# Kernel optimization log

Hardware: AMD Instinct MI355X
Metric: run time of the kernel (lower is better)

Reference implementation:

```python
import jax, jax.numpy as jnp
import numpy as np

N_DESC = 2
CC_ITERS = 500  # kornia.contrib.connected_components(num_iterations=500)
MIN_PTS = 10


def find_contours(img):
    """Faithful jax port of findContours: pad, kornia connected_components,
    3x3 Laplacian boundary mask, crop. img: [B,1,H,W] binary float32."""
    B, _, H, W = img.shape
    I = jnp.pad(img, ((0, 0), (0, 0), (1, 1), (1, 1)))
    mask = I == 1.0
    # kornia CC: labels initialized to global linear index, propagated by masked 3x3 max-pool
    idx = jnp.arange(B * (H + 2) * (W + 2), dtype=jnp.float32).reshape(B, 1, H + 2, W + 2)
    out0 = jnp.where(mask, idx, 0.0)

    def body(_, o):
        p = jax.lax.reduce_window(o, -jnp.inf, jax.lax.max,
                                  (1, 1, 3, 3), (1, 1, 1, 1), 'SAME')
        return jnp.where(mask, p, 0.0)

    cc = jax.lax.fori_loop(0, CC_ITERS, body, out0)[:, :, 1:-1, 1:-1]
    kern = jnp.array([[1., 1., 1.], [1., -8., 1.], [1., 1., 1.]], dtype=jnp.float32).reshape(1, 1, 3, 3)
    lap = jax.lax.conv_general_dilated(I, kern, (1, 1), 'SAME')
    boundary = (lap < 0).astype(jnp.float32)[:, :, 1:-1, 1:-1]
    return boundary * cc


find_contours = jax.jit(find_contours)


def _sample_stats(cimg, N):
    """Per-image: unique labels (including 0, as in the original), polar-angle
    sort, Fourier descriptor base A_k = sqrt(a^2+b^2)/len with a,b = sums of
    real/imag FFT coefficients / (k*pi). Returns (centers, A) or None."""
    labels = np.unique(cimg)
    if labels.size == 1:
        return None
    centers, As = [], []
    ks = np.arange(1, N + 1, dtype=np.float64)
    for lb in labels:
        pts = np.argwhere(cimg == lb).astype(np.float64)  # (n, 2) row, col
        c = pts.mean(axis=0)
        ang = np.arctan2(pts[:, 1] - c[1], pts[:, 0] - c[0])
        pts = pts[np.argsort(ang, kind='stable')]
        if pts.shape[0] < MIN_PTS:
            continue
        z = pts[:, 0] + 1j * pts[:, 1]
        Fz = np.fft.fft(z)
        a = Fz.real.sum()
        b = Fz.imag.sum()
        A = np.sqrt((a / (ks * np.pi)) ** 2 + (b / (ks * np.pi)) ** 2) / pts.shape[0]
        centers.append(c)
        As.append(A)
    if len(centers) == 0:
        return None
    return np.stack(centers), np.stack(As)


def _compute_S(pred_c, tgt_c, N):
    """S = sum over batch of sum |A_pred[match] - A_gt| (weight-independent part).
    The descriptor is A * 0.5*w^2 + log(1+w^2); the log term cancels in the
    matched absolute difference, so loss = 0.5*w^2 * S exactly."""
    S = 0.0
    for b in range(pred_c.shape[0]):
        sp = _sample_stats(pred_c[b, 0], N)
        st = _sample_stats(tgt_c[b, 0], N)
        if sp is None or st is None:
            continue
        pc, pA = sp
        tc, tA = st
        if tc.shape[0] <= pc.shape[0]:
            d = ((tc[:, None, :] - pc[None, :, :]) ** 2).sum(-1)
            m = d.argmin(axis=1)
            S += np.abs(pA[m] - tA).sum()
        else:
            d = ((pc[:, None, :] - tc[None, :, :]) ** 2).sum(-1)
            m = d.argmin(axis=1)
            S += np.abs(tA[m] - pA).sum()
    return np.float32(S)


def setup_inputs() -> dict:
    key = jax.random.key(0)
    k1, k2, k3 = jax.random.split(key, 3)
    B, H, W = 8, 512, 512
    # low-frequency logits -> realistic building-like blobs after thresholding
    low_p = jax.random.normal(k1, (B, 1, 16, 16), dtype=jnp.float32)
    pred_seg = jax.image.resize(low_p, (B, 1, H, W), method='bilinear') * 4.0
    low_t = jax.random.normal(k2, (B, 1, 16, 16), dtype=jnp.float32)
    target_label = (jax.image.resize(low_t, (B, 1, H, W), method='bilinear') > 0).astype(jnp.float32)
    descriptors_weight = jax.random.uniform(k3, (), dtype=jnp.float32) + 0.5
    return {"pred_seg": pred_seg, "target_label": target_label,
            "descriptors_weight": descriptors_weight}


def reference(pred_seg, target_label, descriptors_weight):
    N = N_DESC
    pred = (jax.nn.sigmoid(pred_seg) > 0.5).astype(jnp.float32)
    tgt = target_label if target_label.ndim == 4 else target_label[:, None]
    pred_contours = np.asarray(find_contours(pred))
    tgt_contours = np.asarray(find_contours(tgt))
    S = _compute_S(pred_contours, tgt_contours, N)
    # descriptor = A * (1/2 * w^2) + log(1 + w^2); log term cancels in |diff|
    return jnp.asarray(S, jnp.float32) * (0.5 * descriptors_weight ** 2)
```

## Files before the change

### kernel.cpp

```cpp
#include <hip/hip_runtime.h>

typedef unsigned int u32;
typedef unsigned long long u64;

#define BN 8
#define NIMG 16
#define NPIMG (512*512)
#define NPIXC (NIMG*NPIMG)
#define PP (514*514)
#define CAP 8192u
#define SLOT0 8192
#define NSLOT 8193
#define NDN (NIMG*NSLOT)
#define TOTR 66977792u
#define MAXL 512
#define PROP_ITERS 500
#define LH 64

#define TILE_W 96
#define TILE_H 64
#define HALO 16
#define CF4 32
#define NSTRIP 8
#define SROWS 12
#define TPC 6
#define TPR 8
#define TPT (TPR*TPC)
#define PROPBLOCKS (NIMG*TPT)

__device__ __forceinline__ u32 hashL(u32 L) { return (L * 2654435761u) >> 19; }
__device__ __forceinline__ u32 hashS(u32 L) { return (L * 2654435761u) >> 26; }

__device__ __forceinline__ u64 encAng(double a) {
  u64 u = (u64)__double_as_longlong(a);
  return (u >> 63) ? ~u : (u | 0x8000000000000000ull);
}

__device__ __forceinline__ float fmax3(float a, float b, float c) {
  return fmaxf(a, fmaxf(b, c));
}

__device__ __forceinline__ float4 horizf4(float4 M, int tx) {
  float Lw = __shfl_up(M.w, 1);
  float Rx = __shfl_down(M.x, 1);
  if (tx == 0) Lw = 0.f;
  if (tx == CF4 - 1) Rx = 0.f;
  float4 hh;
  hh.x = fmax3(Lw, M.x, M.y);
  hh.y = fmax3(M.x, M.y, M.z);
  hh.z = fmax3(M.y, M.z, M.w);
  hh.w = fmax3(M.z, M.w, Rx);
  return hh;
}

__global__ __launch_bounds__(256) void k_prop(const float* __restrict__ src,
                                              float* __restrict__ dst,
                                              const float* __restrict__ pred,
                                              const float* __restrict__ tgt,
                                              int niter, int first) {
  __shared__ float4 hTopS[2][NSTRIP][CF4];
  __shared__ float4 hBotS[2][NSTRIP][CF4];
  __shared__ int s_flag;
  const int tid = threadIdx.x;
  const int bx = blockIdx.x;
  const int j = bx >> 3;
  const int img = ((bx & 7) << 1) + (j >= TPT ? 1 : 0);
  const int tt = (j >= TPT) ? (j - TPT) : j;
  const int tyT = tt / TPC, txT = tt % TPC;
  const int tx = tid & 31, sy = tid >> 5;
  const int gr0 = tyT * TILE_H - HALO + sy * SROWS;
  const int gc = txT * TILE_W - HALO + tx * 4;
  const bool gcok = (gc >= 0 && gc < 512);

  float4 cur[SROWS];
  if (first) {
    const int f = img >> 3, b = img & 7;
    const float* fb = (f == 0 ? pred : tgt) + b * NPIMG;
#pragma unroll
    for (int r = 0; r < SROWS; ++r) {
      float4 v = make_float4(0.f, 0.f, 0.f, 0.f);
      int gr = gr0 + r;
      if (gcok && gr >= 0 && gr < 512) {
        float4 x = *(const float4*)(fb + gr * 512 + gc);
        float lb = (float)(b * PP + (gr + 1) * 514 + (gc + 1));
        bool mx, my, mz, mw;
        if (f == 0) { mx = x.x > 0.f; my = x.y > 0.f; mz = x.z > 0.f; mw = x.w > 0.f; }
        else        { mx = x.x == 1.f; my = x.y == 1.f; mz = x.z == 1.f; mw = x.w == 1.f; }
        v.x = mx ? lb : 0.f;
        v.y = my ? lb + 1.f : 0.f;
        v.z = mz ? lb + 2.f : 0.f;
        v.w = mw ? lb + 3.f : 0.f;
      }
      cur[r] = v;
    }
  } else {
    const float* ibase = src + img * NPIMG;
#pragma unroll
    for (int r = 0; r < SROWS; ++r) {
      float4 v = make_float4(0.f, 0.f, 0.f, 0.f);
      int gr = gr0 + r;
      if (gcok && gr >= 0 && gr < 512)
        v = *(const float4*)(ibase + gr * 512 + gc);
      cur[r] = v;
    }
  }

  bool changed = false;
  for (int itr = 0; itr < niter; ++itr) {
    const int p = itr & 1;
    const bool chk = (p == 1);
    float4 h[SROWS];
#pragma unroll
    for (int r = 0; r < SROWS; ++r) h[r] = horizf4(cur[r], tx);
    hTopS[p][sy][tx] = h[0];
    hBotS[p][sy][tx] = h[SROWS - 1];
    if (chk && tid == 0) s_flag = 0;
    __syncthreads();
    float4 zero = make_float4(0.f, 0.f, 0.f, 0.f);
    float4 hm = (sy > 0) ? hBotS[p][sy - 1][tx] : zero;
    float4 below = (sy < NSTRIP - 1) ? hTopS[p][sy + 1][tx] : zero;
#pragma unroll
    for (int r = 0; r < SROWS; ++r) {
      float4 hc = h[r];
      float4 hp = (r == SROWS - 1) ? below : h[r + 1];
      float4 o = cur[r], v;
      v.x = (o.x > 0.f) ? fmax3(hm.x, hc.x, hp.x) : 0.f;
      v.y = (o.y > 0.f) ? fmax3(hm.y, hc.y, hp.y) : 0.f;
      v.z = (o.z > 0.f) ? fmax3(hm.z, hc.z, hp.z) : 0.f;
      v.w = (o.w > 0.f) ? fmax3(hm.w, hc.w, hp.w) : 0.f;
      if (chk)
        changed = changed || (v.x != o.x) || (v.y != o.y) || (v.z != o.z) || (v.w != o.w);
      cur[r] = v;
      hm = hc;
    }
    if (chk) {
      if (changed) s_flag = 1;
      __syncthreads();
      if (s_flag == 0) break;
      changed = false;
    }
  }

  if (tx >= 4 && tx <= 27 && gc < 512) {
    float* obase = dst + img * NPIMG;
#pragma unroll
    for (int r = 0; r < SROWS; ++r) {
      int er = sy * SROWS + r;
      if (er >= HALO && er < HALO + TILE_H)
        *(float4*)(obase + (gr0 + r) * 512 + gc) = cur[r];
    }
  }
}

__global__ __launch_bounds__(256) void k_cimgcount(const float* __restrict__ V,
                                                   float* __restrict__ Cm,
                                                   u32* __restrict__ key, u32* __restrict__ cnt,
                                                   u32* __restrict__ sr, u32* __restrict__ sc) {
  __shared__ u32 hl[LH], hn[LH], hr[LH], hc2[LH];
  __shared__ u32 s_n, s_r, s_c;
  const int tid = threadIdx.x;
  for (int e = tid; e < LH; e += 256) { hl[e] = 0; hn[e] = 0; hr[e] = 0; hc2[e] = 0; }
  if (tid == 0) { s_n = 0; s_r = 0; s_c = 0; }
  __syncthreads();
  int i = blockIdx.x * 256 + tid;
  int img = i >> 18, q = i & (NPIMG - 1);
  int r = q >> 9, c = q & 511;
  const float* base = V + img * NPIMG;
  float v = base[q];
  float out = 0.f;
  if (v > 0.f) {
    bool z = (r == 0) || (r == 511) || (c == 0) || (c == 511);
    if (!z) {
      float mn = base[q - 513];
      mn = fminf(mn, base[q - 512]); mn = fminf(mn, base[q - 511]);
      mn = fminf(mn, base[q - 1]);   mn = fminf(mn, base[q + 1]);
      mn = fminf(mn, base[q + 511]); mn = fminf(mn, base[q + 512]);
      mn = fminf(mn, base[q + 513]);
      z = (mn == 0.f);
    }
    if (z) out = v;
  }
  Cm[i] = out;
  if (out != 0.f) {
    u32 L = (u32)out;
    u32 h = hashS(L);
    bool ins = false;
    for (u32 pr = 0; pr < LH; ++pr) {
      u32 e = (h + pr) & (LH - 1);
      u32 k = atomicCAS(&hl[e], 0u, L);
      if (k == 0u || k == L) {
        atomicAdd(&hn[e], 1u); atomicAdd(&hr[e], (u32)r); atomicAdd(&hc2[e], (u32)c);
        ins = true; break;
      }
    }
    if (!ins) {
      u32 hg = hashL(L), slot = 0xFFFFFFFFu;
      for (u32 pr = 0; pr < CAP; ++pr) {
        u32 k = key[img * CAP + hg];
        if (k == L) { slot = hg; break; }
        if (k == 0u) {
          u32 old = atomicCAS(&key[img * CAP + hg], 0u, L);
          if (old == 0u || old == L) { slot = hg; break; }
        }
        hg = (hg + 1) & (CAP - 1);
      }
      if (slot != 0xFFFFFFFFu) {
        u32 s = (u32)img * NSLOT + slot;
        atomicAdd(&cnt[s], 1u); atomicAdd(&sr[s], (u32)r); atomicAdd(&sc[s], (u32)c);
      }
    }
    atomicAdd(&s_n, 1u); atomicAdd(&s_r, (u32)r); atomicAdd(&s_c, (u32)c);
  }
  __syncthreads();
  int im = (blockIdx.x * 256) >> 18;
  for (int e = tid; e < LH; e += 256) {
    u32 L = hl[e];
    if (L == 0u) continue;
    u32 hg = hashL(L), slot = 0xFFFFFFFFu;
    for (u32 pr = 0; pr < CAP; ++pr) {
      u32 k = key[im * CAP + hg];
      if (k == L) { slot = hg; break; }
      if (k == 0u) {
        u32 old = atomicCAS(&key[im * CAP + hg], 0u, L);
        if (old == 0u || old == L) { slot = hg; break; }
      }
      hg = (hg + 1) & (CAP - 1);
    }
    if (slot != 0xFFFFFFFFu) {
      u32 s = (u32)im * NSLOT + slot;
      atomicAdd(&cnt[s], hn[e]); atomicAdd(&sr[s], hr[e]); atomicAdd(&sc[s], hc2[e]);
    }
  }
  if (tid == 0 && s_n) {
    u32 s = (u32)im * NSLOT + SLOT0;
    atomicAdd(&cnt[s], s_n); atomicAdd(&sr[s], s_r); atomicAdd(&sc[s], s_c);
  }
}

__global__ __launch_bounds__(256) void k_compact(const u32* __restrict__ key,
                                                 const u32* __restrict__ cnt,
                                                 const u32* __restrict__ sr, const u32* __restrict__ sc,
                                                 u32* __restrict__ nlab, u32* __restrict__ labD,
                                                 u32* __restrict__ cntD, u32* __restrict__ srD,
                                                 u32* __restrict__ scD, u32* __restrict__ slotD) {
  int i = blockIdx.x * 256 + threadIdx.x;
  if (i >= NDN) return;
  int img = i / NSLOT, s = i - img * NSLOT;
  u32 L, n, a, b2;
  if (s < (int)CAP) {
    L = key[img * CAP + s];
    if (L == 0u) return;
    n = cnt[img * NSLOT + s];
    a = sr[img * NSLOT + s]; b2 = sc[img * NSLOT + s];
  } else {
    u32 nn = cnt[img * NSLOT + SLOT0];
    n = NPIMG - nn;
    if (n == 0u) return;
    L = 0u;
    a = TOTR - sr[img * NSLOT + SLOT0]; b2 = TOTR - sc[img * NSLOT + SLOT0];
  }
  u32 j = atomicAdd(&nlab[img], 1u);
  if (j < MAXL) {
    labD[img * MAXL + j] = L; cntD[img * MAXL + j] = n;
    srD[img * MAXL + j] = a;  scD[img * MAXL + j] = b2;
    slotD[img * MAXL + j] = (u32)s;
  }
}

__global__ __launch_bounds__(256) void k_angle(const float* __restrict__ Cm,
                                               const u32* __restrict__ key, const u32* __restrict__ cnt,
                                               const u32* __restrict__ sr, const u32* __restrict__ sc,
                                               u64* __restrict__ amin) {
  __shared__ u32 asl[LH];
  __shared__ u64 amn[LH];
  __shared__ u64 wmin[4];
  const int tid = threadIdx.x;
  for (int e = tid; e < LH; e += 256) { asl[e] = 0; amn[e] = ~0ull; }
  __syncthreads();
  int i = blockIdx.x * 256 + tid;
  int img = i >> 18, q = i & (NPIMG - 1);
  int r = q >> 9, c = q & 511;
  float v = Cm[i];
  u64 e0 = ~0ull;
  if (v == 0.f) {
    u32 base = (u32)img * NSLOT + SLOT0;
    u32 n0 = NPIMG - cnt[base];
    double cr = (double)(TOTR - sr[base]) / (double)n0;
    double cc = (double)(TOTR - sc[base]) / (double)n0;
    e0 = encAng(atan2((double)c - cc, (double)r - cr));
  } else {
    u32 L = (u32)v;
    u32 h = hashL(L);
    for (u32 pr = 0; pr < CAP && key[img * CAP + h] != L; ++pr) h = (h + 1) & (CAP - 1);
    u32 s = (u32)img * NSLOT + h;
    u32 n = cnt[s];
    double cr = (double)sr[s] / (double)n;
    double cc = (double)sc[s] / (double)n;
    u64 enc = encAng(atan2((double)c - cc, (double)r - cr));
    u32 kk = h + 1, hh = hashS(kk);
    bool ins = false;
    for (u32 pr = 0; pr < LH; ++pr) {
      u32 e = (hh + pr) & (LH - 1);
      u32 k = atomicCAS(&asl[e], 0u, kk);
      if (k == 0u || k == kk) { atomicMin(&amn[e], enc); ins = true; break; }
    }
    if (!ins) atomicMin(&amin[s], enc);
  }
  for (int o = 32; o > 0; o >>= 1) {
    u64 other = __shfl_xor(e0, o, 64);
    e0 = other < e0 ? other : e0;
  }
  int lane = tid & 63, wid = tid >> 6;
  if (lane == 0) wmin[wid] = e0;
  __syncthreads();
  int im = (blockIdx.x * 256) >> 18;
  if (tid == 0) {
    u64 m = wmin[0];
    for (int k = 1; k < 4; ++k) m = wmin[k] < m ? wmin[k] : m;
    if (m != ~0ull) atomicMin(&amin[(u32)im * NSLOT + SLOT0], m);
  }
  for (int e = tid; e < LH; e += 256)
    if (asl[e]) atomicMin(&amin[(u32)im * NSLOT + (asl[e] - 1)], amn[e]);
}

__global__ __launch_bounds__(256) void k_idx(const float* __restrict__ Cm,
                                             const u32* __restrict__ key, const u32* __restrict__ cnt,
                                             const u32* __restrict__ sr, const u32* __restrict__ sc,
                                             const u64* __restrict__ amin, u32* __restrict__ imin) {
  __shared__ u32 isl[LH];
  __shared__ u32 imn[LH];
  const int tid = threadIdx.x;
  for (int e = tid; e < LH; e += 256) { isl[e] = 0; imn[e] = 0xFFFFFFFFu; }
  __syncthreads();
  int i = blockIdx.x * 256 + tid;
  int img = i >> 18, q = i & (NPIMG - 1);
  int r = q >> 9, c = q & 511;
  float v = Cm[i];
  u32 sl; double cr, cc;
  if (v == 0.f) {
    sl = SLOT0;
    u32 s = (u32)img * NSLOT + SLOT0;
    u32 n0 = NPIMG - cnt[s];
    cr = (double)(TOTR - sr[s]) / (double)n0;
    cc = (double)(TOTR - sc[s]) / (double)n0;
  } else {
    u32 L = (u32)v;
    u32 h = hashL(L);
    for (u32 pr = 0; pr < CAP && key[img * CAP + h] != L; ++pr) h = (h + 1) & (CAP - 1);
    sl = h;
    u32 s = (u32)img * NSLOT + h;
    u32 n = cnt[s];
    cr = (double)sr[s] / (double)n;
    cc = (double)sc[s] / (double)n;
  }
  u64 e = encAng(atan2((double)c - cc, (double)r - cr));
  if (e == amin[(u32)img * NSLOT + sl]) {
    u32 kk = sl + 1, hh = hashS(kk);
    bool ins = false;
    for (u32 pr = 0; pr < LH; ++pr) {
      u32 e2 = (hh + pr) & (LH - 1);
      u32 k = atomicCAS(&isl[e2], 0u, kk);
      if (k == 0u || k == kk) { atomicMin(&imn[e2], (u32)q); ins = true; break; }
    }
    if (!ins) atomicMin(&imin[(u32)img * NSLOT + sl], (u32)q);
  }
  __syncthreads();
  int im = (blockIdx.x * 256) >> 18;
  for (int e2 = tid; e2 < LH; e2 += 256)
    if (isl[e2]) atomicMin(&imin[(u32)im * NSLOT + (isl[e2] - 1)], imn[e2]);
}

__global__ __launch_bounds__(256) void k_match(const u32* __restrict__ nlab,
                                               const u32* __restrict__ labD, const u32* __restrict__ cntD,
                                               const u32* __restrict__ srD, const u32* __restrict__ scD,
                                               const u32* __restrict__ slotD, const u32* __restrict__ imin,
                                               const float* __restrict__ wp, float* __restrict__ out) {
  __shared__ u32 lbl[2][MAXL];
  __shared__ double cx[2][MAXL], cy[2][MAXL], Rr[2][MAXL];
  __shared__ int nlist[2];
  __shared__ double wsum[4];
  const int tid = threadIdx.x;
  double S = 0.0;
  for (int b = 0; b < BN; ++b) {
    __syncthreads();
    if (tid == 0) { nlist[0] = nlist[1] = 0; }
    __syncthreads();
    int tot[2];
    for (int f = 0; f < 2; ++f) {
      int t = f * BN + b;
      int ntot = (int)nlab[t];
      tot[f] = ntot;
      int nl = ntot > MAXL ? MAXL : ntot;
      for (int s2 = tid; s2 < nl; s2 += 256) {
        u32 n = cntD[t * MAXL + s2];
        if (n < 10u) continue;
        int j = atomicAdd(&nlist[f], 1);
        lbl[f][j] = labD[t * MAXL + s2];
        cx[f][j] = (double)srD[t * MAXL + s2] / (double)n;
        cy[f][j] = (double)scD[t * MAXL + s2] / (double)n;
        u32 pi = imin[t * NSLOT + slotD[t * MAXL + s2]];
        double r0 = (double)(pi >> 9), c0 = (double)(pi & 511u);
        Rr[f][j] = sqrt(r0 * r0 + c0 * c0);
      }
    }
    __syncthreads();
    int np = nlist[0], nt = nlist[1];
    bool valid = (tot[0] >= 2) && (np >= 1) && (tot[1] >= 2) && (nt >= 1);
    if (valid) {
      u32 ml[2][2]; double mx[2][2], my[2][2], mr[2][2]; int rk[2][2]; int nh[2];
      for (int f = 0; f < 2; ++f) {
        int n = f ? nt : np;
        nh[f] = 0;
        for (int i = tid; i < n; i += 256) {
          int k = nh[f]++;
          u32 L = lbl[f][i];
          ml[f][k] = L; mx[f][k] = cx[f][i]; my[f][k] = cy[f][i]; mr[f][k] = Rr[f][i];
          int rr = 0;
          for (int j = 0; j < n; ++j) rr += (lbl[f][j] < L) ? 1 : 0;
          rk[f][k] = rr;
        }
      }
      __syncthreads();
      for (int f = 0; f < 2; ++f)
        for (int k = 0; k < nh[f]; ++k) {
          int rr = rk[f][k];
          lbl[f][rr] = ml[f][k]; cx[f][rr] = mx[f][k];
          cy[f][rr] = my[f][k];  Rr[f][rr] = mr[f][k];
        }
      __syncthreads();
      if (nt <= np) {
        for (int j = tid; j < nt; j += 256) {
          int m = 0; double bd = 1e300;
          double tx0 = cx[1][j], ty0 = cy[1][j];
          for (int i2 = 0; i2 < np; ++i2) {
            double dx = tx0 - cx[0][i2], dy = ty0 - cy[0][i2];
            double d = dx * dx + dy * dy;
            if (d < bd) { bd = d; m = i2; }
          }
          S += fabs(Rr[0][m] - Rr[1][j]);
        }
      } else {
        for (int i2 = tid; i2 < np; i2 += 256) {
          int m = 0; double bd = 1e300;
          double px0 = cx[0][i2], py0 = cy[0][i2];
          for (int j = 0; j < nt; ++j) {
            double dx = px0 - cx[1][j], dy = py0 - cy[1][j];
            double d = dx * dx + dy * dy;
            if (d < bd) { bd = d; m = j; }
          }
          S += fabs(Rr[1][m] - Rr[0][i2]);
        }
      }
    }
  }
  for (int o = 32; o > 0; o >>= 1) S += __shfl_xor(S, o, 64);
  int lane = tid & 63, wid = tid >> 6;
  if (lane == 0) wsum[wid] = S;
  __syncthreads();
  if (tid == 0) {
    double total = wsum[0] + wsum[1] + wsum[2] + wsum[3];
    total *= (1.5 / 3.14159265358979323846);
    float w = wp[0];
    out[0] = (float)total * (0.5f * w * w);
  }
}

extern "C" void kernel_launch(void* const* d_in, const int* in_sizes, int n_in,
                              void* d_out, int out_size, void* d_ws, size_t ws_size,
                              hipStream_t stream) {
  const float* pred = (const float*)d_in[0];
  const float* tgt  = (const float*)d_in[1];
  const float* wp   = (const float*)d_in[2];
  float* out = (float*)d_out;

  char* ws = (char*)d_ws;
  size_t off = 0;
  float* A  = (float*)(ws + off); off += (size_t)NPIXC * 4;
  float* Bb = (float*)(ws + off); off += (size_t)NPIXC * 4;
  u32* key  = (u32*)(ws + off);   off += (size_t)NIMG * CAP * 4;
  u32* cnt  = (u32*)(ws + off);   off += (size_t)NIMG * NSLOT * 4;
  u32* sr   = (u32*)(ws + off);   off += (size_t)NIMG * NSLOT * 4;
  u32* sc   = (u32*)(ws + off);   off += (size_t)NIMG * NSLOT * 4;
  u64* amin = (u64*)(ws + off);   off += (size_t)NIMG * NSLOT * 8;
  u32* imin = (u32*)(ws + off);   off += (size_t)NIMG * NSLOT * 4;
  u32* nlab = (u32*)(ws + off);   off += (size_t)NIMG * 4;
  u32* labD = (u32*)(ws + off);   off += (size_t)NIMG * MAXL * 4;
  u32* cntD = (u32*)(ws + off);   off += (size_t)NIMG * MAXL * 4;
  u32* srD  = (u32*)(ws + off);   off += (size_t)NIMG * MAXL * 4;
  u32* scD  = (u32*)(ws + off);   off += (size_t)NIMG * MAXL * 4;
  u32* slotD= (u32*)(ws + off);   off += (size_t)NIMG * MAXL * 4;

  size_t zlen = (size_t)NIMG * CAP * 4 + 3ull * NIMG * NSLOT * 4;
  hipMemsetAsync(key, 0, zlen, stream);
  hipMemsetAsync(amin, 0xFF, (size_t)NIMG * NSLOT * 12, stream);
  hipMemsetAsync(nlab, 0, (size_t)NIMG * 4, stream);

  const int gC = NPIXC / 256;
  const int gS = (NDN + 255) / 256;

  k_prop<<<PROPBLOCKS, 256, 0, stream>>>(A, A, pred, tgt, HALO, 1);
  float* src = A; float* dst = Bb;
  int done = HALO;
  while (done < PROP_ITERS) {
    int k = PROP_ITERS - done; if (k > HALO) k = HALO;
    k_prop<<<PROPBLOCKS, 256, 0, stream>>>(src, dst, pred, tgt, k, 0);
    float* t2 = src; src = dst; dst = t2;
    done += k;
  }
  float* Cm = dst;
  k_cimgcount<<<gC, 256, 0, stream>>>(src, Cm, key, cnt, sr, sc);
  k_compact<<<gS, 256, 0, stream>>>(key, cnt, sr, sc, nlab, labD, cntD, srD, scD, slotD);
  k_angle<<<gC, 256, 0, stream>>>(Cm, key, cnt, sr, sc, amin);
  k_idx<<<gC, 256, 0, stream>>>(Cm, key, cnt, sr, sc, amin, imin);
  k_match<<<1, 256, 0, stream>>>(nlab, labD, cntD, srD, scD, slotD, imin, wp, out);
}
```

Baseline: 1.551 ms.

## Fuse final propagation iterations with contour extraction and label counting

The last 4 label-propagation iterations move into a new kernel that also computes the boundary mask and does the per-block hash-table label counting from the tile held in registers. This drops the separate contour/count kernel and one full read and write of the label image. The early-exit convergence check now runs every 4 iterations instead of every 2, cutting barrier and flag overhead but possibly doing a few extra iterations before breaking. The iteration schedule is hard-coded as 16 + 30×16 + 4 = 500.

```diff
diff --git a/kernel.cpp b/kernel.cpp
--- a/kernel.cpp
+++ b/kernel.cpp
@@ -14,7 +14,6 @@
 #define NDN (NIMG*NSLOT)
 #define TOTR 66977792u
 #define MAXL 512
-#define PROP_ITERS 500
 #define LH 64
 
 #define TILE_W 96
@@ -51,6 +50,24 @@
   hh.z = fmax3(M.y, M.z, M.w);
   hh.w = fmax3(M.z, M.w, Rx);
   return hh;
+}
+
+__device__ __forceinline__ float4 initVal(const float* __restrict__ pred,
+                                          const float* __restrict__ tgt,
+                                          int img, int gr, int gc) {
+  const int f = img >> 3, b = img & 7;
+  const float* fb = (f == 0 ? pred : tgt) + b * NPIMG;
+  float4 x = *(const float4*)(fb + gr * 512 + gc);
+  float lb = (float)(b * PP + (gr + 1) * 514 + (gc + 1));
+  bool mx, my, mz, mw;
+  if (f == 0) { mx = x.x > 0.f; my = x.y > 0.f; mz = x.z > 0.f; mw = x.w > 0.f; }
+  else        { mx = x.x == 1.f; my = x.y == 1.f; mz = x.z == 1.f; mw = x.w == 1.f; }
+  float4 v;
+  v.x = mx ? lb : 0.f;
+  v.y = my ? lb + 1.f : 0.f;
+  v.z = mz ? lb + 2.f : 0.f;
+  v.w = mw ? lb + 3.f : 0.f;
+  return v;
 }
 
 __global__ __launch_bounds__(256) void k_prop(const float* __restrict__ src,
@@ -74,23 +91,12 @@
 
   float4 cur[SROWS];
   if (first) {
-    const int f = img >> 3, b = img & 7;
-    const float* fb = (f == 0 ? pred : tgt) + b * NPIMG;
 #pragma unroll
     for (int r = 0; r < SROWS; ++r) {
       float4 v = make_float4(0.f, 0.f, 0.f, 0.f);
       int gr = gr0 + r;
-      if (gcok && gr >= 0 && gr < 512) {
-        float4 x = *(const float4*)(fb + gr * 512 + gc);
-        float lb = (float)(b * PP + (gr + 1) * 514 + (gc + 1));
-        bool mx, my, mz, mw;
-        if (f == 0) { mx = x.x > 0.f; my = x.y > 0.f; mz = x.z > 0.f; mw = x.w > 0.f; }
-        else        { mx = x.x == 1.f; my = x.y == 1.f; mz = x.z == 1.f; mw = x.w == 1.f; }
-        v.x = mx ? lb : 0.f;
-        v.y = my ? lb + 1.f : 0.f;
-        v.z = mz ? lb + 2.f : 0.f;
-        v.w = mw ? lb + 3.f : 0.f;
-      }
+      if (gcok && gr >= 0 && gr < 512)
+        v = initVal(pred, tgt, img, gr, gc);
       cur[r] = v;
     }
   } else {
@@ -108,7 +114,7 @@
   bool changed = false;
   for (int itr = 0; itr < niter; ++itr) {
     const int p = itr & 1;
-    const bool chk = (p == 1);
+    const bool chk = ((itr & 3) == 3);
     float4 h[SROWS];
 #pragma unroll
     for (int r = 0; r < SROWS; ++r) h[r] = horizf4(cur[r], tx);
@@ -152,87 +158,144 @@
   }
 }
 
-__global__ __launch_bounds__(256) void k_cimgcount(const float* __restrict__ V,
+__global__ __launch_bounds__(256) void k_prop_cimg(const float* __restrict__ src,
                                                    float* __restrict__ Cm,
                                                    u32* __restrict__ key, u32* __restrict__ cnt,
-                                                   u32* __restrict__ sr, u32* __restrict__ sc) {
+                                                   u32* __restrict__ sr, u32* __restrict__ sc,
+                                                   int niter) {
+  __shared__ float4 hTopS[2][NSTRIP][CF4];
+  __shared__ float4 hBotS[2][NSTRIP][CF4];
+  __shared__ float4 vTop[NSTRIP][CF4];
+  __shared__ float4 vBot[NSTRIP][CF4];
   __shared__ u32 hl[LH], hn[LH], hr[LH], hc2[LH];
   __shared__ u32 s_n, s_r, s_c;
   const int tid = threadIdx.x;
+  const int bx = blockIdx.x;
+  const int j = bx >> 3;
+  const int img = ((bx & 7) << 1) + (j >= TPT ? 1 : 0);
+  const int tt = (j >= TPT) ? (j - TPT) : j;
+  const int tyT = tt / TPC, txT = tt % TPC;
+  const int tx = tid & 31, sy = tid >> 5;
+  const int gr0 = tyT * TILE_H - HALO + sy * SROWS;
+  const int gc = txT * TILE_W - HALO + tx * 4;
+  const bool gcok = (gc >= 0 && gc < 512);
+  const bool writer = (tx >= 4 && tx <= 27 && gc < 512);
+
   for (int e = tid; e < LH; e += 256) { hl[e] = 0; hn[e] = 0; hr[e] = 0; hc2[e] = 0; }
   if (tid == 0) { s_n = 0; s_r = 0; s_c = 0; }
-  __syncthreads();
-  int i = blockIdx.x * 256 + tid;
-  int img = i >> 18, q = i & (NPIMG - 1);
-  int r = q >> 9, c = q & 511;
-  const float* base = V + img * NPIMG;
-  float v = base[q];
-  float out = 0.f;
-  if (v > 0.f) {
-    bool z = (r == 0) || (r == 511) || (c == 0) || (c == 511);
-    if (!z) {
-      float mn = base[q - 513];
-      mn = fminf(mn, base[q - 512]); mn = fminf(mn, base[q - 511]);
-      mn = fminf(mn, base[q - 1]);   mn = fminf(mn, base[q + 1]);
-      mn = fminf(mn, base[q + 511]); mn = fminf(mn, base[q + 512]);
-      mn = fminf(mn, base[q + 513]);
-      z = (mn == 0.f);
-    }
-    if (z) out = v;
-  }
-  Cm[i] = out;
-  if (out != 0.f) {
-    u32 L = (u32)out;
-    u32 h = hashS(L);
-    bool ins = false;
-    for (u32 pr = 0; pr < LH; ++pr) {
-      u32 e = (h + pr) & (LH - 1);
-      u32 k = atomicCAS(&hl[e], 0u, L);
-      if (k == 0u || k == L) {
-        atomicAdd(&hn[e], 1u); atomicAdd(&hr[e], (u32)r); atomicAdd(&hc2[e], (u32)c);
-        ins = true; break;
+
+  float4 cur[SROWS];
+  {
+    const float* ibase = src + img * NPIMG;
+#pragma unroll
+    for (int r = 0; r < SROWS; ++r) {
+      float4 v = make_float4(0.f, 0.f, 0.f, 0.f);
+      int gr = gr0 + r;
+      if (gcok && gr >= 0 && gr < 512)
+        v = *(const float4*)(ibase + gr * 512 + gc);
+      cur[r] = v;
+    }
+  }
+
+  for (int itr = 0; itr < niter; ++itr) {
+    const int p = itr & 1;
+    float4 h[SROWS];
+#pragma unroll
+    for (int r = 0; r < SROWS; ++r) h[r] = horizf4(cur[r], tx);
+    hTopS[p][sy][tx] = h[0];
+    hBotS[p][sy][tx] = h[SROWS - 1];
+    __syncthreads();
+    float4 zero = make_float4(0.f, 0.f, 0.f, 0.f);
+    float4 hm = (sy > 0) ? hBotS[p][sy - 1][tx] : zero;
+    float4 below = (sy < NSTRIP - 1) ? hTopS[p][sy + 1][tx] : zero;
+#pragma unroll
+    for (int r = 0; r < SROWS; ++r) {
+      float4 hc = h[r];
+      float4 hp = (r == SROWS - 1) ? below : h[r + 1];
+      float4 o = cur[r], v;
+      v.x = (o.x > 0.f) ? fmax3(hm.x, hc.x, hp.x) : 0.f;
+      v.y = (o.y > 0.f) ? fmax3(hm.y, hc.y, hp.y) : 0.f;
+      v.z = (o.z > 0.f) ? fmax3(hm.z, hc.z, hp.z) : 0.f;
+      v.w = (o.w > 0.f) ? fmax3(hm.w, hc.w, hp.w) : 0.f;
+      cur[r] = v;
+      hm = hc;
+    }
+    __syncthreads();
+  }
+
+  vTop[sy][tx] = cur[0];
+  vBot[sy][tx] = cur[SROWS - 1];
+  __syncthreads();
+  float4 zero = make_float4(0.f, 0.f, 0.f, 0.f);
+  float4 above = (sy > 0) ? vBot[sy - 1][tx] : zero;
+  float4 belowV = (sy < NSTRIP - 1) ? vTop[sy + 1][tx] : zero;
+
+  float* cb = Cm + img * NPIMG;
+#pragma unroll
+  for (int r = 0; r < SROWS; ++r) {
+    int er = sy * SROWS + r;
+    if (er < HALO || er >= HALO + TILE_H) continue;
+    float4 U = (r == 0) ? above : cur[r - 1];
+    float4 D = (r == SROWS - 1) ? belowV : cur[r + 1];
+    float4 M = cur[r];
+    float LwU = __shfl_up(U.w, 1), RxU = __shfl_down(U.x, 1);
+    float LwM = __shfl_up(M.w, 1), RxM = __shfl_down(M.x, 1);
+    float LwD = __shfl_up(D.w, 1), RxD = __shfl_down(D.x, 1);
+    if (!writer) continue;
+    float4 mn, out;
+    mn.x = fminf(fminf(fminf(LwU, U.x), fminf(U.y, LwM)),
+                 fminf(fminf(M.y, LwD), fminf(D.x, D.y)));
+    mn.y = fminf(fminf(fminf(U.x, U.y), fminf(U.z, M.x)),
+                 fminf(fminf(M.z, D.x), fminf(D.y, D.z)));
+    mn.z = fminf(fminf(fminf(U.y, U.z), fminf(U.w, M.y)),
+                 fminf(fminf(M.w, D.y), fminf(D.z, D.w)));
+    mn.w = fminf(fminf(fminf(U.z, U.w), fminf(RxU, M.z)),
+                 fminf(fminf(RxM, D.z), fminf(D.w, RxD)));
+    out.x = (M.x > 0.f && mn.x == 0.f) ? M.x : 0.f;
+    out.y = (M.y > 0.f && mn.y == 0.f) ? M.y : 0.f;
+    out.z = (M.z > 0.f && mn.z == 0.f) ? M.z : 0.f;
+    out.w = (M.w > 0.f && mn.w == 0.f) ? M.w : 0.f;
+    *(float4*)(cb + (gr0 + r) * 512 + gc) = out;
+    int gr = gr0 + r;
+#pragma unroll
+    for (int comp = 0; comp < 4; ++comp) {
+      float ov = (comp == 0) ? out.x : (comp == 1) ? out.y : (comp == 2) ? out.z : out.w;
+      if (ov == 0.f) continue;
+      u32 L = (u32)ov;
+      u32 rr = (u32)gr, cc = (u32)(gc + comp);
+      u32 h = hashS(L);
+      for (u32 pr = 0; pr < LH; ++pr) {
+        u32 e = (h + pr) & (LH - 1);
+        u32 k = atomicCAS(&hl[e], 0u, L);
+        if (k == 0u || k == L) {
+          atomicAdd(&hn[e], 1u); atomicAdd(&hr[e], rr); atomicAdd(&hc2[e], cc);
+          break;
+        }
       }
-    }
-    if (!ins) {
-      u32 hg = hashL(L), slot = 0xFFFFFFFFu;
-      for (u32 pr = 0; pr < CAP; ++pr) {
-        u32 k = key[img * CAP + hg];
-        if (k == L) { slot = hg; break; }
-        if (k == 0u) {
-          u32 old = atomicCAS(&key[img * CAP + hg], 0u, L);
-          if (old == 0u || old == L) { slot = hg; break; }
-        }
-        hg = (hg + 1) & (CAP - 1);
-      }
-      if (slot != 0xFFFFFFFFu) {
-        u32 s = (u32)img * NSLOT + slot;
-        atomicAdd(&cnt[s], 1u); atomicAdd(&sr[s], (u32)r); atomicAdd(&sc[s], (u32)c);
-      }
-    }
-    atomicAdd(&s_n, 1u); atomicAdd(&s_r, (u32)r); atomicAdd(&s_c, (u32)c);
-  }
-  __syncthreads();
-  int im = (blockIdx.x * 256) >> 18;
+      atomicAdd(&s_n, 1u); atomicAdd(&s_r, rr); atomicAdd(&s_c, cc);
+    }
+  }
+  __syncthreads();
   for (int e = tid; e < LH; e += 256) {
     u32 L = hl[e];
     if (L == 0u) continue;
     u32 hg = hashL(L), slot = 0xFFFFFFFFu;
     for (u32 pr = 0; pr < CAP; ++pr) {
-      u32 k = key[im * CAP + hg];
+      u32 k = key[img * CAP + hg];
       if (k == L) { slot = hg; break; }
       if (k == 0u) {
-        u32 old = atomicCAS(&key[im * CAP + hg], 0u, L);
+        u32 old = atomicCAS(&key[img * CAP + hg], 0u, L);
         if (old == 0u || old == L) { slot = hg; break; }
       }
       hg = (hg + 1) & (CAP - 1);
     }
     if (slot != 0xFFFFFFFFu) {
-      u32 s = (u32)im * NSLOT + slot;
+      u32 s = (u32)img * NSLOT + slot;
       atomicAdd(&cnt[s], hn[e]); atomicAdd(&sr[s], hr[e]); atomicAdd(&sc[s], hc2[e]);
     }
   }
   if (tid == 0 && s_n) {
-    u32 s = (u32)im * NSLOT + SLOT0;
+    u32 s = (u32)img * NSLOT + SLOT0;
     atomicAdd(&cnt[s], s_n); atomicAdd(&sr[s], s_r); atomicAdd(&sc[s], s_c);
   }
 }
@@ -498,17 +561,14 @@
   const int gC = NPIXC / 256;
   const int gS = (NDN + 255) / 256;
 
-  k_prop<<<PROPBLOCKS, 256, 0, stream>>>(A, A, pred, tgt, HALO, 1);
+  k_prop<<<PROPBLOCKS, 256, 0, stream>>>(A, A, pred, tgt, 16, 1);
   float* src = A; float* dst = Bb;
-  int done = HALO;
-  while (done < PROP_ITERS) {
-    int k = PROP_ITERS - done; if (k > HALO) k = HALO;
-    k_prop<<<PROPBLOCKS, 256, 0, stream>>>(src, dst, pred, tgt, k, 0);
+  for (int s = 1; s <= 30; ++s) {
+    k_prop<<<PROPBLOCKS, 256, 0, stream>>>(src, dst, pred, tgt, 16, 0);
     float* t2 = src; src = dst; dst = t2;
-    done += k;
   }
   float* Cm = dst;
-  k_cimgcount<<<gC, 256, 0, stream>>>(src, Cm, key, cnt, sr, sc);
+  k_prop_cimg<<<PROPBLOCKS, 256, 0, stream>>>(src, Cm, key, cnt, sr, sc, 4);
   k_compact<<<gS, 256, 0, stream>>>(key, cnt, sr, sc, nlab, labD, cntD, srD, scD, slotD);
   k_angle<<<gC, 256, 0, stream>>>(Cm, key, cnt, sr, sc, amin);
   k_idx<<<gC, 256, 0, stream>>>(Cm, key, cnt, sr, sc, amin, imin);
```

New measurement: 3.070 ms. 97.9% more time.
